# Optimization experiments

Hardware: AMD Instinct MI355X
Metric: run time of the kernel (lower is better)

The kernel has to match this reference:

```python
import jax, jax.numpy as jnp
from jax import lax
import numpy as np

B, DM, NL, NC = 4, 256, 4, 1000
DI, NS, DTR, K = 512, 16, 32, 4  # d_inner, d_state, dt_rank, d_conv
EPS = 1e-5


def _bn(x, g, b):
    # eval-mode BatchNorm2d with running stats (mean=0, var=1)
    return x * (g / jnp.sqrt(1.0 + EPS))[None, :, None, None] + b[None, :, None, None]


def _conv2d(x, w, b, stride, pad):
    y = lax.conv_general_dilated(x, w, (stride, stride), pad,
                                 dimension_numbers=('NCHW', 'OIHW', 'NCHW'))
    return y + b[None, :, None, None]


def _ln(x, g, b):
    m = x.mean(-1, keepdims=True)
    v = ((x - m) ** 2).mean(-1, keepdims=True)
    return (x - m) / jnp.sqrt(v + EPS) * g + b


def _selective_scan(u, delta, A, Bm, Cm, D):
    # u, delta: [b,d,l]; A: [d,n]; Bm, Cm: [b,n,l]; D: [d]
    dA = jnp.exp(jnp.einsum('bdl,dn->lbdn', delta, A))        # [l,b,d,n]
    dBu = jnp.einsum('bdl,bnl,bdl->lbdn', delta, Bm, u)       # [l,b,d,n]
    h0 = jnp.zeros(dA.shape[1:], u.dtype)

    def step(h, inp):
        a, bu = inp
        h = a * h + bu
        return h, h

    _, hs = lax.scan(step, h0, (dA, dBu))                     # [l,b,d,n]
    y = jnp.einsum('lbdn,bnl->bdl', hs, Cm)
    return y + u * D[None, :, None]


def _mamba_block(x, ipw, ipb, cw, cb, xpw, dpw, dpb, alog, dssm, opw, opb):
    # x: [b,l,d_model]
    xr = x @ ipw.T + ipb                                      # [b,l,2*DI]
    xi, res = jnp.split(xr, 2, axis=-1)
    xc = jnp.swapaxes(xi, 1, 2)                               # [b,DI,l]
    # depthwise conv1d, kernel 4, torch padding='same' -> pad (1,2)
    xc = lax.conv_general_dilated(xc, cw, (1,), [(1, 2)],
                                  dimension_numbers=('NCW', 'OIW', 'NCW'),
                                  feature_group_count=DI) + cb[None, :, None]
    xl = jnp.swapaxes(xc, 1, 2)                               # [b,l,DI]
    xdbl = xl @ xpw.T                                         # [b,l,DTR+2*NS]
    d_dt, Bs, Cs = jnp.split(xdbl, [DTR, DTR + NS], axis=-1)
    delta = jax.nn.softplus(d_dt @ dpw.T + dpb)               # [b,l,DI]
    A = -jnp.exp(alog)                                        # [DI,NS]
    y = _selective_scan(jnp.swapaxes(xl, 1, 2), jnp.swapaxes(delta, 1, 2), A,
                        jnp.swapaxes(Bs, 1, 2), jnp.swapaxes(Cs, 1, 2), dssm)
    y = jnp.swapaxes(y, 1, 2)                                 # [b,l,DI]
    y = y * jax.nn.silu(res)
    return y @ opw.T + opb


def setup_inputs() -> dict:
    key = jax.random.key(0)
    ks = iter(jax.random.split(key, 32))

    def rn(shape, scale=0.02):
        return jax.random.normal(next(ks), shape, jnp.float32) * scale

    inp = {
        'x': jax.random.normal(next(ks), (B, 3, 64, 64), jnp.float32),
        # conv stem
        'c1w': rn((DM // 2, 3, 3, 3)), 'c1b': jnp.zeros((DM // 2,)),
        'g1': jnp.ones((DM // 2,)), 'b1': jnp.zeros((DM // 2,)),
        'c2w': rn((DM, DM // 2, 3, 3)), 'c2b': jnp.zeros((DM,)),
        'g2': jnp.ones((DM,)), 'b2': jnp.zeros((DM,)),
        'pw': rn((DM, DM, 2, 2)), 'pb': jnp.zeros((DM,)),
        'g3': jnp.ones((DM,)), 'b3': jnp.zeros((DM,)),
        # stacked mamba block params [NL, ...]
        'ipw': rn((NL, 2 * DI, DM)), 'ipb': jnp.zeros((NL, 2 * DI)),
        'cw': rn((NL, DI, 1, K), 0.1), 'cb': jnp.zeros((NL, DI)),
        'xpw': rn((NL, DTR + 2 * NS, DI)),
        'dpw': rn((NL, DI, DTR)), 'dpb': rn((NL, DI), 0.1),
        'alog': jnp.broadcast_to(jnp.log(jnp.arange(1, NS + 1, dtype=jnp.float32)), (NL, DI, NS)),
        'dssm': jnp.ones((NL, DI)),
        'opw': rn((NL, DM, DI)), 'opb': jnp.zeros((NL, DM)),
        'lnw': jnp.ones((NL, DM)), 'lnb': jnp.zeros((NL, DM)),
        # head
        'nw': jnp.ones((DM,)), 'nb': jnp.zeros((DM,)),
        'fcw': rn((NC, DM)), 'fcb': jnp.zeros((NC,)),
    }
    return inp


def reference(x, c1w, c1b, g1, b1, c2w, c2b, g2, b2, pw, pb, g3, b3,
              ipw, ipb, cw, cb, xpw, dpw, dpb, alog, dssm, opw, opb,
              lnw, lnb, nw, nb, fcw, fcb):
    h = _conv2d(x, c1w, c1b, 1, [(1, 1), (1, 1)])
    h = jax.nn.gelu(_bn(h, g1, b1), approximate=False)
    h = _conv2d(h, c2w, c2b, 1, [(1, 1), (1, 1)])
    h = jax.nn.gelu(_bn(h, g2, b2), approximate=False)
    h = _conv2d(h, pw, pb, 2, [(0, 0), (0, 0)])
    h = jax.nn.gelu(_bn(h, g3, b3), approximate=False)
    b, c, H, W = h.shape
    s = h.reshape(b, c, H * W).transpose(0, 2, 1)             # [b, L, d_model]
    for i in range(NL):
        y = _mamba_block(s, ipw[i], ipb[i], cw[i], cb[i], xpw[i], dpw[i],
                         dpb[i], alog[i], dssm[i], opw[i], opb[i])
        s = _ln(y, lnw[i], lnb[i]) + s
    s = s.mean(axis=1)
    s = _ln(s, nw, nb)
    logits = s @ fcw.T + fcb
    return logits, jax.nn.softmax(logits, axis=-1)
```

## Files before the change

kernel.cpp:

```cpp
#include <hip/hip_runtime.h>
#include <math.h>


#define BN_RSQ 0.99999500003749969f

typedef unsigned int uint;
typedef unsigned short ushort;
typedef __bf16 bf16x8 __attribute__((ext_vector_type(8)));
typedef float floatx4 __attribute__((ext_vector_type(4)));

__device__ __forceinline__ float gelu_f(float v) {
    return 0.5f * v * (1.0f + erff(v * 0.70710678118654752f));
}
__device__ __forceinline__ float softplus_f(float v) {
    return (v > 20.f) ? v : log1pf(expf(v));
}
__device__ __forceinline__ ushort f2bf(float f) {
    uint x = __float_as_uint(f);
    x += 0x7fffu + ((x >> 16) & 1u);
    return (ushort)(x >> 16);
}
__device__ __forceinline__ float bf2f(ushort u) {
    return __uint_as_float((uint)u << 16);
}

__global__ void wprep(const float* __restrict__ ipw, const float* __restrict__ opw,
                      const float* __restrict__ c2w, const float* __restrict__ pw,
                      const float* __restrict__ xpw,
                      ushort* __restrict__ ipwb, ushort* __restrict__ opwb,
                      ushort* __restrict__ w2b, ushort* __restrict__ pwTb,
                      ushort* __restrict__ xpwb)
{
    int idx = blockIdx.x * 256 + threadIdx.x;
    if (idx < 1048576) {
        ipwb[idx] = f2bf(ipw[idx]);
    } else if (idx < 1572864) {
        int i = idx - 1048576;
        opwb[i] = f2bf(opw[i]);
    } else if (idx < 1867776) {
        int i = idx - 1572864;
        int oc = i / 1152, k = i % 1152;
        int s = k >> 7, ic = k & 127;
        w2b[i] = f2bf(c2w[(size_t)(oc * 128 + ic) * 9 + s]);
    } else if (idx < 2129920) {
        int i = idx - 1867776;
        int oc = i >> 10, k = i & 1023;
        int s = k >> 8, ic = k & 255;
        int ky = s >> 1, kx = s & 1;
        pwTb[i] = f2bf(pw[((size_t)(oc * 256 + ic) * 2 + ky) * 2 + kx]);
    } else if (idx < 2260992) {
        int i = idx - 2129920;
        xpwb[i] = f2bf(xpw[i]);
    }
}

__global__ __launch_bounds__(256) void conv1_nhwc(
    const float* __restrict__ x, const float* __restrict__ w,
    const float* __restrict__ cb, const float* __restrict__ g,
    const float* __restrict__ bb, ushort* __restrict__ out)
{
    __shared__ float tin[3][3][64];
    __shared__ float ws[3456];
    int t = threadIdx.x;
    int b = blockIdx.x >> 6, y = blockIdx.x & 63;
    for (int i = t; i < 3456; i += 256) ws[i] = w[i];
    for (int i = t; i < 576; i += 256) {
        int ic = i / 192, r = (i >> 6) % 3, xx = i & 63;
        int gy = y + r - 1;
        tin[ic][r][xx] = ((unsigned)gy < 64u) ? x[((b * 3 + ic) * 64 + gy) * 64 + xx] : 0.f;
    }
    __syncthreads();
    int tx = t & 15, ty = t >> 4;
    int oc0 = tx * 8, px0 = ty * 4;
    float acc[4][8];
    #pragma unroll
    for (int p = 0; p < 4; ++p)
        #pragma unroll
        for (int o = 0; o < 8; ++o) acc[p][o] = 0.f;
    for (int ic = 0; ic < 3; ++ic)
        #pragma unroll
        for (int ky = 0; ky < 3; ++ky)
            #pragma unroll
            for (int kx = 0; kx < 3; ++kx) {
                float av[4];
                #pragma unroll
                for (int p = 0; p < 4; ++p) {
                    int xx = px0 + p + kx - 1;
                    av[p] = ((unsigned)xx < 64u) ? tin[ic][ky][xx] : 0.f;
                }
                #pragma unroll
                for (int o = 0; o < 8; ++o) {
                    float wv = ws[(oc0 + o) * 27 + ic * 9 + ky * 3 + kx];
                    #pragma unroll
                    for (int p = 0; p < 4; ++p) acc[p][o] = fmaf(av[p], wv, acc[p][o]);
                }
            }
    #pragma unroll
    for (int p = 0; p < 4; ++p) {
        uint pk[4];
        #pragma unroll
        for (int o2 = 0; o2 < 4; ++o2) {
            int oc = oc0 + o2 * 2;
            float v0 = gelu_f((acc[p][o2 * 2] + cb[oc]) * (g[oc] * BN_RSQ) + bb[oc]);
            float v1 = gelu_f((acc[p][o2 * 2 + 1] + cb[oc + 1]) * (g[oc + 1] * BN_RSQ) + bb[oc + 1]);
            pk[o2] = (uint)f2bf(v0) | ((uint)f2bf(v1) << 16);
        }
        uint4 vv = make_uint4(pk[0], pk[1], pk[2], pk[3]);
        *(uint4*)(out + ((size_t)((b * 64 + y) * 64 + px0 + p)) * 128 + oc0) = vv;
    }
}

template<int BM, int BN, int EPI>
__global__ __launch_bounds__(256, 2) void mfma_gemm_bt(
    const ushort* __restrict__ A, int lda,
    const ushort* __restrict__ W, int ldw,
    const float* __restrict__ bias,
    const float* __restrict__ bnG, const float* __restrict__ bnB,
    float* __restrict__ Cf, ushort* __restrict__ Cb, ushort* __restrict__ Cb2,
    int ldc, int K)
{
    constexpr int PAD = 40;
    constexpr int AP = BM / 64;
    constexpr int BP = BN / 64;
    constexpr int FM = BM / 32;
    constexpr int FN = BN / 32;
    __shared__ __align__(16) ushort As[BM * PAD];
    __shared__ __align__(16) ushort Bs[BN * PAD];
    int t = threadIdx.x;
    int m0 = blockIdx.x * BM, n0 = blockIdx.y * BN;
    int lane = t & 63, wid = t >> 6;
    int wm = (wid & 1) * (BM / 2), wn = (wid >> 1) * (BN / 2);
    int fr = lane & 15, fk = (lane >> 4) * 8;
    int r0 = t >> 2, c0 = (t & 3) * 8;
    floatx4 acc[FM][FN];
    #pragma unroll
    for (int i = 0; i < FM; ++i)
        #pragma unroll
        for (int j = 0; j < FN; ++j) acc[i][j] = {0.f, 0.f, 0.f, 0.f};
    uint4 ra[AP], rb[BP];
    #pragma unroll
    for (int p = 0; p < AP; ++p)
        ra[p] = *(const uint4*)(A + (size_t)(m0 + r0 + p * 64) * lda + c0);
    #pragma unroll
    for (int p = 0; p < BP; ++p)
        rb[p] = *(const uint4*)(W + (size_t)(n0 + r0 + p * 64) * ldw + c0);
    for (int k0 = 0; k0 < K; k0 += 32) {
        __syncthreads();
        #pragma unroll
        for (int p = 0; p < AP; ++p) *(uint4*)&As[(r0 + p * 64) * PAD + c0] = ra[p];
        #pragma unroll
        for (int p = 0; p < BP; ++p) *(uint4*)&Bs[(r0 + p * 64) * PAD + c0] = rb[p];
        __syncthreads();
        if (k0 + 32 < K) {
            #pragma unroll
            for (int p = 0; p < AP; ++p)
                ra[p] = *(const uint4*)(A + (size_t)(m0 + r0 + p * 64) * lda + k0 + 32 + c0);
            #pragma unroll
            for (int p = 0; p < BP; ++p)
                rb[p] = *(const uint4*)(W + (size_t)(n0 + r0 + p * 64) * ldw + k0 + 32 + c0);
        }
        bf16x8 af[FM], bw[FN];
        #pragma unroll
        for (int i = 0; i < FM; ++i)
            af[i] = *(const bf16x8*)&As[(wm + i * 16 + fr) * PAD + fk];
        #pragma unroll
        for (int j = 0; j < FN; ++j)
            bw[j] = *(const bf16x8*)&Bs[(wn + j * 16 + fr) * PAD + fk];
        #pragma unroll
        for (int i = 0; i < FM; ++i)
            #pragma unroll
            for (int j = 0; j < FN; ++j)
                acc[i][j] = __builtin_amdgcn_mfma_f32_16x16x32_bf16(af[i], bw[j], acc[i][j], 0, 0, 0);
    }
    int rbase = (lane >> 4) * 4, cc = lane & 15;
    #pragma unroll
    for (int j = 0; j < FN; ++j) {
        int n = n0 + wn + j * 16 + cc;
        float bv = bias ? bias[n] : 0.f;
        float scl = 0.f, shf = 0.f;
        if (EPI == 2) { scl = bnG[n] * BN_RSQ; shf = bnB[n]; }
        #pragma unroll
        for (int i = 0; i < FM; ++i) {
            #pragma unroll
            for (int r = 0; r < 4; ++r) {
                int m = m0 + wm + i * 16 + rbase + r;
                float v = acc[i][j][r] + bv;
                if (EPI == 2) v = gelu_f(v * scl + shf);
                if (EPI == 0) {
                    Cf[(size_t)m * ldc + n] = v;
                } else if (EPI == 2) {
                    Cf[(size_t)m * ldc + n] = v;
                    Cb[(size_t)m * ldc + n] = f2bf(v);
                } else {
                    if (n < 512) Cb[(size_t)m * 512 + n] = f2bf(v);
                    else Cb2[(size_t)m * 512 + (n - 512)] = f2bf(v / (1.f + __expf(-v)));
                }
            }
        }
    }
}

#define C2_LOAD(step)                                                            \
    {                                                                            \
        int s_ = (step) >> 1, ich_ = ((step) & 1) * 64;                          \
        int ky_ = s_ / 3, kx_ = s_ % 3;                                          \
        int sy_ = y0 + (ra_row >> 6) + ky_ - 1;                                  \
        int sx_ = (ra_row & 63) + kx_ - 1;                                       \
        bool v_ = ((unsigned)sy_ < 64u) && ((unsigned)sx_ < 64u);                \
        const ushort* ap_ = hb + ((size_t)(sy_ * 64 + sx_)) * 128 + ich_ + ra_c; \
        uint4 zz_ = make_uint4(0u, 0u, 0u, 0u);                                  \
        ra0 = v_ ? *(const uint4*)(ap_ + 0)  : zz_;                              \
        ra1 = v_ ? *(const uint4*)(ap_ + 8)  : zz_;                              \
        ra2 = v_ ? *(const uint4*)(ap_ + 16) : zz_;                              \
        ra3 = v_ ? *(const uint4*)(ap_ + 24) : zz_;                              \
        const ushort* wp_ = w2b + (size_t)(n0 + rb_row) * 1152 + s_ * 128 + ich_ + rb_c; \
        rb0 = *(const uint4*)(wp_ + 0);                                          \
        rb1 = *(const uint4*)(wp_ + 8);                                          \
    }

__global__ __launch_bounds__(256, 2) void conv2_mfma(
    const ushort* __restrict__ h1b, const ushort* __restrict__ w2b,
    const float* __restrict__ cb, const float* __restrict__ g,
    const float* __restrict__ bb, ushort* __restrict__ h2b)
{
    constexpr int PAD = 72;
    __shared__ __align__(16) ushort As[128 * PAD];
    __shared__ __align__(16) ushort Bs[64 * PAD];
    int t = threadIdx.x;
    int m0 = blockIdx.x * 128, n0 = blockIdx.y * 64;
    int b = m0 >> 12;
    int y0 = (m0 & 4095) >> 6;
    int lane = t & 63, wid = t >> 6;
    int wm = (wid & 1) * 64, wn = (wid >> 1) * 32;
    int fr = lane & 15, fk = (lane >> 4) * 8;
    int ra_row = t >> 1, ra_c = (t & 1) * 32;
    int rb_row = t >> 2, rb_c = (t & 3) * 16;
    floatx4 acc[4][2];
    #pragma unroll
    for (int i = 0; i < 4; ++i)
        #pragma unroll
        for (int j = 0; j < 2; ++j) acc[i][j] = {0.f, 0.f, 0.f, 0.f};
    const ushort* hb = h1b + (size_t)b * 4096 * 128;

    uint4 ra0, ra1, ra2, ra3, rb0, rb1;
    C2_LOAD(0);
    for (int step = 0; step < 18; ++step) {
        __syncthreads();
        *(uint4*)&As[ra_row * PAD + ra_c + 0]  = ra0;
        *(uint4*)&As[ra_row * PAD + ra_c + 8]  = ra1;
        *(uint4*)&As[ra_row * PAD + ra_c + 16] = ra2;
        *(uint4*)&As[ra_row * PAD + ra_c + 24] = ra3;
        *(uint4*)&Bs[rb_row * PAD + rb_c + 0]  = rb0;
        *(uint4*)&Bs[rb_row * PAD + rb_c + 8]  = rb1;
        __syncthreads();
        if (step + 1 < 18) C2_LOAD(step + 1);
        #pragma unroll
        for (int ks = 0; ks < 64; ks += 32) {
            bf16x8 af[4], bw[2];
            #pragma unroll
            for (int i = 0; i < 4; ++i)
                af[i] = *(const bf16x8*)&As[(wm + i * 16 + fr) * PAD + ks + fk];
            #pragma unroll
            for (int j = 0; j < 2; ++j)
                bw[j] = *(const bf16x8*)&Bs[(wn + j * 16 + fr) * PAD + ks + fk];
            #pragma unroll
            for (int i = 0; i < 4; ++i)
                #pragma unroll
                for (int j = 0; j < 2; ++j)
                    acc[i][j] = __builtin_amdgcn_mfma_f32_16x16x32_bf16(af[i], bw[j], acc[i][j], 0, 0, 0);
        }
    }
    int rbase = (lane >> 4) * 4, cc = lane & 15;
    #pragma unroll
    for (int j = 0; j < 2; ++j) {
        int n = n0 + wn + j * 16 + cc;
        float scl = g[n] * BN_RSQ, shf = bb[n], bv2 = cb[n];
        #pragma unroll
        for (int i = 0; i < 4; ++i) {
            #pragma unroll
            for (int r = 0; r < 4; ++r) {
                int m = m0 + wm + i * 16 + rbase + r;
                float v = gelu_f((acc[i][j][r] + bv2) * scl + shf);
                h2b[(size_t)m * 256 + n] = f2bf(v);
            }
        }
    }
}

__global__ void im2col_bf16(const ushort* __restrict__ h2b, ushort* __restrict__ Apb)
{
    int idx = blockIdx.x * 256 + threadIdx.x;
    int k8 = idx & 127;
    int m = idx >> 7;
    int b = m >> 10, oy = (m >> 5) & 31, ox = m & 31;
    int s = k8 >> 5, ic8 = k8 & 31;
    int ky = s >> 1, kx = s & 1;
    uint4 v = *(const uint4*)(h2b + ((size_t)(b * 4096 + (2 * oy + ky) * 64 + 2 * ox + kx)) * 256 + ic8 * 8);
    *(uint4*)(Apb + (size_t)m * 1024 + k8 * 8) = v;
}

template<int BM, int BN, int BK, int TM, int TN>
__global__ __launch_bounds__(256) void gemm_kernel(
    const float* __restrict__ A, int lda,
    const float* __restrict__ W, int ldw,
    const float* __restrict__ bias,
    float* __restrict__ C, int ldc,
    int M, int N, int K, int act)
{
    static_assert(BM * BK / 4 == 256 && BN * BK / 4 == 256, "staging shape");
    __shared__ float As[BK][BM + 4];
    __shared__ float Bs[BK][BN + 4];
    int t = threadIdx.x;
    int m0 = blockIdx.x * BM, n0 = blockIdx.y * BN;
    float acc[TM][TN];
    #pragma unroll
    for (int i = 0; i < TM; i++)
        #pragma unroll
        for (int j = 0; j < TN; j++) acc[i][j] = 0.f;
    const int LPR = BK / 4;
    int lr = t / LPR, lc4 = (t % LPR) * 4;
    int ty = t >> 4, tx = t & 15;
    int ma = m0 + lr, nb = n0 + lr;
    float4 va = make_float4(0.f, 0.f, 0.f, 0.f);
    float4 vb = make_float4(0.f, 0.f, 0.f, 0.f);
    if (ma < M) va = *(const float4*)(A + (size_t)ma * lda + lc4);
    if (nb < N) vb = *(const float4*)(W + (size_t)nb * ldw + lc4);
    for (int k0 = 0; k0 < K; k0 += BK) {
        __syncthreads();
        As[lc4 + 0][lr] = va.x; As[lc4 + 1][lr] = va.y;
        As[lc4 + 2][lr] = va.z; As[lc4 + 3][lr] = va.w;
        Bs[lc4 + 0][lr] = vb.x; Bs[lc4 + 1][lr] = vb.y;
        Bs[lc4 + 2][lr] = vb.z; Bs[lc4 + 3][lr] = vb.w;
        __syncthreads();
        if (k0 + BK < K) {
            if (ma < M) va = *(const float4*)(A + (size_t)ma * lda + k0 + BK + lc4);
            if (nb < N) vb = *(const float4*)(W + (size_t)nb * ldw + k0 + BK + lc4);
        }
        #pragma unroll
        for (int kk = 0; kk < BK; ++kk) {
            float a[TM], bfr[TN];
            #pragma unroll
            for (int i = 0; i < TM; i += 4)
                *(float4*)&a[i] = *(const float4*)&As[kk][ty * TM + i];
            #pragma unroll
            for (int j = 0; j < TN; j += 4)
                *(float4*)&bfr[j] = *(const float4*)&Bs[kk][tx * TN + j];
            #pragma unroll
            for (int i = 0; i < TM; i++)
                #pragma unroll
                for (int j = 0; j < TN; j++) acc[i][j] = fmaf(a[i], bfr[j], acc[i][j]);
        }
    }
    #pragma unroll
    for (int i = 0; i < TM; i++) {
        int m = m0 + ty * TM + i;
        if (m >= M) continue;
        #pragma unroll
        for (int j = 0; j < TN; j++) {
            int n = n0 + tx * TN + j;
            if (n >= N) continue;
            float v = acc[i][j];
            if (bias) v += bias[n];
            if (act == 2) v = softplus_f(v);
            C[(size_t)m * ldc + n] = v;
        }
    }
}

__global__ __launch_bounds__(256) void dwconv(
    const ushort* __restrict__ xib, const float* __restrict__ cw,
    const float* __restrict__ cb, float* __restrict__ xl, ushort* __restrict__ xlb)
{
    int idx = blockIdx.x * 256 + threadIdx.x;
    int d4 = (idx & 127) * 4;
    int bl = idx >> 7;
    int b = bl >> 10, l = bl & 1023;
    float4 w0 = *(const float4*)(cw + d4 * 4);
    float4 w1 = *(const float4*)(cw + d4 * 4 + 4);
    float4 w2 = *(const float4*)(cw + d4 * 4 + 8);
    float4 w3 = *(const float4*)(cw + d4 * 4 + 12);
    float4 acc = *(const float4*)(cb + d4);
    const ushort* rowb = xib + ((size_t)b << 19) + d4;
    #pragma unroll
    for (int k = 0; k < 4; ++k) {
        int ll = l + k - 1;
        if ((unsigned)ll < 1024u) {
            uint2 p = *(const uint2*)(rowb + (size_t)ll * 512);
            acc.x = fmaf(bf2f((ushort)(p.x & 0xffffu)), ((const float*)&w0)[k], acc.x);
            acc.y = fmaf(bf2f((ushort)(p.x >> 16)),     ((const float*)&w1)[k], acc.y);
            acc.z = fmaf(bf2f((ushort)(p.y & 0xffffu)), ((const float*)&w2)[k], acc.z);
            acc.w = fmaf(bf2f((ushort)(p.y >> 16)),     ((const float*)&w3)[k], acc.w);
        }
    }
    *(float4*)(xl + (size_t)bl * 512 + d4) = acc;
    uint2 pk;
    pk.x = (uint)f2bf(acc.x) | ((uint)f2bf(acc.y) << 16);
    pk.y = (uint)f2bf(acc.z) | ((uint)f2bf(acc.w) << 16);
    *(uint2*)(xlb + (size_t)bl * 512 + d4) = pk;
}

__global__ __launch_bounds__(512) void scan_part1(
    const float* __restrict__ delta, const float* __restrict__ u,
    const float* __restrict__ xdbl, const float* __restrict__ alog,
    float* __restrict__ Psum, float* __restrict__ hFsum)
{
    __shared__ float Td[32][132];
    __shared__ float Tu[32][132];
    __shared__ float TB[16][132];
    int t = threadIdx.x;
    int bid = blockIdx.x;
    int ch = bid & 7, dgG = (bid >> 3) & 15, b = bid >> 7;
    int d0 = dgG * 32;
    int bl0 = b * 1024 + ch * 128;
    #pragma unroll
    for (int r = 0; r < 2; ++r) {
        int idx = r * 512 + t;
        int l = idx >> 3, d4 = (idx & 7) * 4;
        float4 dv = *(const float4*)(delta + (size_t)(bl0 + l) * 512 + d0 + d4);
        float4 uv = *(const float4*)(u + (size_t)(bl0 + l) * 512 + d0 + d4);
        Td[d4 + 0][l] = dv.x; Td[d4 + 1][l] = dv.y; Td[d4 + 2][l] = dv.z; Td[d4 + 3][l] = dv.w;
        Tu[d4 + 0][l] = uv.x; Tu[d4 + 1][l] = uv.y; Tu[d4 + 2][l] = uv.z; Tu[d4 + 3][l] = uv.w;
    }
    {
        int l = t >> 2, n4 = (t & 3) * 4;
        float4 bv = *(const float4*)(xdbl + (size_t)(bl0 + l) * 64 + 32 + n4);
        TB[n4 + 0][l] = bv.x; TB[n4 + 1][l] = bv.y; TB[n4 + 2][l] = bv.z; TB[n4 + 3][l] = bv.w;
    }
    __syncthreads();
    int w = t >> 6, lane = t & 63;
    int dl = lane >> 4, n = lane & 15;
    int col = w * 4 + dl;
    int d = d0 + col;
    float Ac = -__expf(alog[d * 16 + n]);
    float h = 0.f, P = 1.f;
    for (int l4 = 0; l4 < 32; ++l4) {
        float4 de = *(const float4*)&Td[col][l4 * 4];
        float4 uu = *(const float4*)&Tu[col][l4 * 4];
        float4 Bv = *(const float4*)&TB[n][l4 * 4];
        float a;
        a = __expf(de.x * Ac); h = a * h + de.x * Bv.x * uu.x; P *= a;
        a = __expf(de.y * Ac); h = a * h + de.y * Bv.y * uu.y; P *= a;
        a = __expf(de.z * Ac); h = a * h + de.z * Bv.z * uu.z; P *= a;
        a = __expf(de.w * Ac); h = a * h + de.w * Bv.w * uu.w; P *= a;
    }
    size_t si = ((size_t)(b * 128 + dgG * 8 + w) * 8 + ch) * 64 + lane;
    Psum[si] = P;
    hFsum[si] = h;
}

__global__ __launch_bounds__(512) void scan_part2(
    const float* __restrict__ delta, const float* __restrict__ u,
    const float* __restrict__ xdbl,
    const float* __restrict__ alog, const float* __restrict__ dssm,
    const ushort* __restrict__ resb, ushort* __restrict__ ybb,
    const float* __restrict__ Psum, const float* __restrict__ hFsum)
{
    __shared__ float Td[32][132];
    __shared__ float Tu[32][132];
    __shared__ float TB[16][132];
    __shared__ float TC[16][132];
    __shared__ float yb[128][33];
    int t = threadIdx.x;
    int bid = blockIdx.x;
    int ch = bid & 7, dgG = (bid >> 3) & 15, b = bid >> 7;
    int d0 = dgG * 32;
    int bl0 = b * 1024 + ch * 128;
    #pragma unroll
    for (int r = 0; r < 2; ++r) {
        int idx = r * 512 + t;
        int l = idx >> 3, d4 = (idx & 7) * 4;
        float4 dv = *(const float4*)(delta + (size_t)(bl0 + l) * 512 + d0 + d4);
        float4 uv = *(const float4*)(u + (size_t)(bl0 + l) * 512 + d0 + d4);
        Td[d4 + 0][l] = dv.x; Td[d4 + 1][l] = dv.y; Td[d4 + 2][l] = dv.z; Td[d4 + 3][l] = dv.w;
        Tu[d4 + 0][l] = uv.x; Tu[d4 + 1][l] = uv.y; Tu[d4 + 2][l] = uv.z; Tu[d4 + 3][l] = uv.w;
    }
    {
        int l = t >> 2, n4 = (t & 3) * 4;
        float4 bv = *(const float4*)(xdbl + (size_t)(bl0 + l) * 64 + 32 + n4);
        float4 cv = *(const float4*)(xdbl + (size_t)(bl0 + l) * 64 + 48 + n4);
        TB[n4 + 0][l] = bv.x; TB[n4 + 1][l] = bv.y; TB[n4 + 2][l] = bv.z; TB[n4 + 3][l] = bv.w;
        TC[n4 + 0][l] = cv.x; TC[n4 + 1][l] = cv.y; TC[n4 + 2][l] = cv.z; TC[n4 + 3][l] = cv.w;
    }
    __syncthreads();
    int w = t >> 6, lane = t & 63;
    int dl = lane >> 4, n = lane & 15;
    int col = w * 4 + dl;
    int d = d0 + col;
    float Ac = -__expf(alog[d * 16 + n]);
    float Dd = dssm[d];
    float h = 0.f;
    {
        size_t sbase = (size_t)(b * 128 + dgG * 8 + w) * 512 + lane;
        for (int cc = 0; cc < ch; ++cc) {
            float Pv = Psum[sbase + (size_t)cc * 64];
            float hv = hFsum[sbase + (size_t)cc * 64];
            h = Pv * h + hv;
        }
    }
    for (int l4 = 0; l4 < 32; ++l4) {
        float4 de = *(const float4*)&Td[col][l4 * 4];
        float4 uu = *(const float4*)&Tu[col][l4 * 4];
        float4 Bv = *(const float4*)&TB[n][l4 * 4];
        float4 Cv = *(const float4*)&TC[n][l4 * 4];
        float p0, p1, p2, p3;
        h = __expf(de.x * Ac) * h + de.x * Bv.x * uu.x; p0 = h * Cv.x;
        h = __expf(de.y * Ac) * h + de.y * Bv.y * uu.y; p1 = h * Cv.y;
        h = __expf(de.z * Ac) * h + de.z * Bv.z * uu.z; p2 = h * Cv.z;
        h = __expf(de.w * Ac) * h + de.w * Bv.w * uu.w; p3 = h * Cv.w;
        #pragma unroll
        for (int off = 1; off < 16; off <<= 1) {
            p0 += __shfl_xor(p0, off);
            p1 += __shfl_xor(p1, off);
            p2 += __shfl_xor(p2, off);
            p3 += __shfl_xor(p3, off);
        }
        if (n == 0) {
            int l = l4 * 4;
            yb[l + 0][col] = fmaf(uu.x, Dd, p0);
            yb[l + 1][col] = fmaf(uu.y, Dd, p1);
            yb[l + 2][col] = fmaf(uu.z, Dd, p2);
            yb[l + 3][col] = fmaf(uu.w, Dd, p3);
        }
    }
    __syncthreads();
    size_t base = ((size_t)(b * 1024 + ch * 128)) * 512 + d0;
    const uint* rp32 = (const uint*)(resb + base);
    uint* yp32 = (uint*)(ybb + base);
    #pragma unroll
    for (int j = 0; j < 4; ++j) {
        int idx = j * 512 + t;
        int l = idx >> 4, du = idx & 15;
        float v0 = yb[l][du * 2 + 0];
        float v1 = yb[l][du * 2 + 1];
        uint rr = rp32[(size_t)l * 256 + du];
        float y0 = v0 * bf2f((ushort)(rr & 0xffffu));
        float y1 = v1 * bf2f((ushort)(rr >> 16));
        yp32[(size_t)l * 256 + du] = (uint)f2bf(y0) | ((uint)f2bf(y1) << 16);
    }
}

__global__ __launch_bounds__(256) void ln_res_kernel(
    const float* __restrict__ o, const float* __restrict__ g,
    const float* __restrict__ bb, float* __restrict__ s, ushort* __restrict__ sb)
{
    int row = blockIdx.x * 4 + (threadIdx.x >> 6);
    int lane = threadIdx.x & 63;
    const float4* orow = (const float4*)(o + (size_t)row * 256);
    float4 v = orow[lane];
    float sum = v.x + v.y + v.z + v.w;
    float sq = v.x * v.x + v.y * v.y + v.z * v.z + v.w * v.w;
    #pragma unroll
    for (int off = 1; off < 64; off <<= 1) {
        sum += __shfl_xor(sum, off);
        sq += __shfl_xor(sq, off);
    }
    float m = sum * (1.f / 256.f);
    float var = sq * (1.f / 256.f) - m * m;
    float rstd = rsqrtf(var + 1e-5f);
    float4 gg = ((const float4*)g)[lane];
    float4 bv = ((const float4*)bb)[lane];
    float4* srow = (float4*)(s + (size_t)row * 256);
    float4 sv = srow[lane];
    sv.x += (v.x - m) * rstd * gg.x + bv.x;
    sv.y += (v.y - m) * rstd * gg.y + bv.y;
    sv.z += (v.z - m) * rstd * gg.z + bv.z;
    sv.w += (v.w - m) * rstd * gg.w + bv.w;
    srow[lane] = sv;
    uint2 pk;
    pk.x = (uint)f2bf(sv.x) | ((uint)f2bf(sv.y) << 16);
    pk.y = (uint)f2bf(sv.z) | ((uint)f2bf(sv.w) << 16);
    *(uint2*)(sb + (size_t)row * 256 + lane * 4) = pk;
}

__global__ __launch_bounds__(256) void pool_ln_kernel(
    const float* __restrict__ s, const float* __restrict__ nw,
    const float* __restrict__ nb, float* __restrict__ sln)
{
    int b = blockIdx.x, c = threadIdx.x;
    const float* p = s + (size_t)b * 262144 + c;
    float acc = 0.f;
    for (int l = 0; l < 1024; ++l) acc += p[(size_t)l * 256];
    float pooled = acc * (1.f / 1024.f);
    __shared__ float rs[4], rq[4];
    float sum = pooled, sq = pooled * pooled;
    #pragma unroll
    for (int off = 1; off < 64; off <<= 1) {
        sum += __shfl_xor(sum, off);
        sq += __shfl_xor(sq, off);
    }
    int w = threadIdx.x >> 6;
    if ((threadIdx.x & 63) == 0) { rs[w] = sum; rq[w] = sq; }
    __syncthreads();
    sum = rs[0] + rs[1] + rs[2] + rs[3];
    sq = rq[0] + rq[1] + rq[2] + rq[3];
    float m = sum * (1.f / 256.f);
    float var = sq * (1.f / 256.f) - m * m;
    float rstd = rsqrtf(var + 1e-5f);
    sln[b * 256 + c] = (pooled - m) * rstd * nw[c] + nb[c];
}

__global__ __launch_bounds__(256) void softmax_kernel(float* __restrict__ out)
{
    int b = threadIdx.x >> 6, lane = threadIdx.x & 63;
    const float* lg = out + b * 1000;
    float v[16];
    float mx = -1e30f;
    #pragma unroll
    for (int j = 0; j < 16; ++j) {
        int i = lane + j * 64;
        v[j] = (i < 1000) ? lg[i] : -1e30f;
        mx = fmaxf(mx, v[j]);
    }
    #pragma unroll
    for (int off = 1; off < 64; off <<= 1) mx = fmaxf(mx, __shfl_xor(mx, off));
    float sum = 0.f;
    #pragma unroll
    for (int j = 0; j < 16; ++j) {
        int i = lane + j * 64;
        if (i < 1000) { v[j] = __expf(v[j] - mx); sum += v[j]; }
    }
    #pragma unroll
    for (int off = 1; off < 64; off <<= 1) sum += __shfl_xor(sum, off);
    float inv = 1.f / sum;
    float* so = out + 4000 + b * 1000;
    #pragma unroll
    for (int j = 0; j < 16; ++j) {
        int i = lane + j * 64;
        if (i < 1000) so[i] = v[j] * inv;
    }
}

extern "C" void kernel_launch(void* const* d_in, const int* in_sizes, int n_in,
                              void* d_out, int out_size, void* d_ws, size_t ws_size,
                              hipStream_t stream)
{
    const float* x    = (const float*)d_in[0];
    const float* c1w  = (const float*)d_in[1];
    const float* c1b  = (const float*)d_in[2];
    const float* g1   = (const float*)d_in[3];
    const float* b1   = (const float*)d_in[4];
    const float* c2w  = (const float*)d_in[5];
    const float* c2b  = (const float*)d_in[6];
    const float* g2   = (const float*)d_in[7];
    const float* b2   = (const float*)d_in[8];
    const float* pw   = (const float*)d_in[9];
    const float* pb   = (const float*)d_in[10];
    const float* g3   = (const float*)d_in[11];
    const float* b3   = (const float*)d_in[12];
    const float* ipw  = (const float*)d_in[13];
    const float* ipb  = (const float*)d_in[14];
    const float* cw   = (const float*)d_in[15];
    const float* cb   = (const float*)d_in[16];
    const float* xpw  = (const float*)d_in[17];
    const float* dpw  = (const float*)d_in[18];
    const float* dpb  = (const float*)d_in[19];
    const float* alog = (const float*)d_in[20];
    const float* dssm = (const float*)d_in[21];
    const float* opw  = (const float*)d_in[22];
    const float* opb  = (const float*)d_in[23];
    const float* lnw  = (const float*)d_in[24];
    const float* lnb  = (const float*)d_in[25];
    const float* nw   = (const float*)d_in[26];
    const float* nb   = (const float*)d_in[27];
    const float* fcw  = (const float*)d_in[28];
    const float* fcb  = (const float*)d_in[29];
    float* out = (float*)d_out;
    float* wsf = (float*)d_ws;

    float*  s_   = wsf;
    ushort* sb   = (ushort*)(wsf + 1048576);
    ushort* xib  = (ushort*)(wsf + 1572864);
    ushort* h2b  = (ushort*)(wsf + 1572864);
    float*  delta= wsf + 1572864;
    float*  obuf = wsf + 1572864;
    ushort* resb = (ushort*)(wsf + 3670016);
    ushort* xlb  = (ushort*)(wsf + 4718592);
    ushort* ybb  = (ushort*)(wsf + 4718592);
    ushort* h1b  = (ushort*)(wsf + 4718592);
    float*  xl   = wsf + 6815744;
    ushort* Apb  = (ushort*)(wsf + 6815744);
    float*  xdbl = wsf + 8912896;
    ushort* ipwb = (ushort*)(wsf + 9175040);
    ushort* opwb = (ushort*)(wsf + 9699328);
    ushort* w2b  = (ushort*)(wsf + 9961472);
    ushort* pwTb = (ushort*)(wsf + 10108928);
    float*  sln  = wsf + 10240000;
    float*  Psum = wsf + 10241024;
    float*  hFsum= wsf + 10503168;
    ushort* xpwb = (ushort*)(wsf + 10765312);

    hipLaunchKernelGGL(wprep, dim3(8832), dim3(256), 0, stream,
                       ipw, opw, c2w, pw, xpw, ipwb, opwb, w2b, pwTb, xpwb);

    hipLaunchKernelGGL(conv1_nhwc, dim3(256), dim3(256), 0, stream, x, c1w, c1b, g1, b1, h1b);
    hipLaunchKernelGGL(conv2_mfma, dim3(128, 4), dim3(256), 0, stream, h1b, w2b, c2b, g2, b2, h2b);
    hipLaunchKernelGGL(im2col_bf16, dim3(2048), dim3(256), 0, stream, h2b, Apb);
    hipLaunchKernelGGL((mfma_gemm_bt<64, 64, 2>), dim3(64, 4), dim3(256), 0, stream,
                       Apb, 1024, pwTb, 1024, pb, g3, b3, s_, sb, nullptr, 256, 1024);

    for (int i = 0; i < 4; ++i) {
        const ushort* ipwb_i = ipwb + (size_t)i * 1024 * 256;
        const float*  ipb_i  = ipb + i * 1024;
        const float*  cw_i   = cw + i * 512 * 4;
        const float*  cb_i   = cb + i * 512;
        const ushort* xpwb_i = xpwb + (size_t)i * 64 * 512;
        const float*  dpw_i  = dpw + (size_t)i * 512 * 32;
        const float*  dpb_i  = dpb + i * 512;
        const float*  alog_i = alog + (size_t)i * 512 * 16;
        const float*  dssm_i = dssm + i * 512;
        const ushort* opwb_i = opwb + (size_t)i * 256 * 512;
        const float*  opb_i  = opb + i * 256;
        const float*  lnw_i  = lnw + i * 256;
        const float*  lnb_i  = lnb + i * 256;

        hipLaunchKernelGGL((mfma_gemm_bt<64, 128, 3>), dim3(64, 8), dim3(256), 0, stream,
                           sb, 256, ipwb_i, 256, ipb_i, nullptr, nullptr,
                           nullptr, xib, resb, 0, 256);
        hipLaunchKernelGGL(dwconv, dim3(2048), dim3(256), 0, stream, xib, cw_i, cb_i, xl, xlb);
        hipLaunchKernelGGL((mfma_gemm_bt<64, 64, 0>), dim3(64, 1), dim3(256), 0, stream,
                           xlb, 512, xpwb_i, 512, nullptr, nullptr, nullptr,
                           xdbl, nullptr, nullptr, 64, 512);
        hipLaunchKernelGGL((gemm_kernel<64, 64, 16, 4, 4>), dim3(64, 8), dim3(256), 0, stream,
                           xdbl, 64, dpw_i, 32, dpb_i, delta, 512, 4096, 512, 32, 2);
        hipLaunchKernelGGL(scan_part1, dim3(512), dim3(512), 0, stream,
                           delta, xl, xdbl, alog_i, Psum, hFsum);
        hipLaunchKernelGGL(scan_part2, dim3(512), dim3(512), 0, stream,
                           delta, xl, xdbl, alog_i, dssm_i, resb, ybb, Psum, hFsum);
        hipLaunchKernelGGL((mfma_gemm_bt<64, 64, 0>), dim3(64, 4), dim3(256), 0, stream,
                           ybb, 512, opwb_i, 512, opb_i, nullptr, nullptr,
                           obuf, nullptr, nullptr, 256, 512);
        hipLaunchKernelGGL(ln_res_kernel, dim3(1024), dim3(256), 0, stream,
                           obuf, lnw_i, lnb_i, s_, sb);
    }

    hipLaunchKernelGGL(pool_ln_kernel, dim3(4), dim3(256), 0, stream, s_, nw, nb, sln);
    hipLaunchKernelGGL((gemm_kernel<64, 64, 16, 4, 4>), dim3(1, 16), dim3(256), 0, stream,
                       sln, 256, fcw, 256, fcb, out, 1000, 4, 1000, 256, 0);
    hipLaunchKernelGGL(softmax_kernel, dim3(1), dim3(256), 0, stream, out);
}
```

Before: 670.1 us.

## Fuse dt_proj GEMM and softplus into scan kernels and read u as bf16

Drops the separate dt_proj GEMM that wrote a float delta tensor. Both scan kernels now recompute delta per tile from xdbl and dpw held in shared memory, then apply softplus. The scan input u is read from the bf16 conv output instead of a float copy, so dwconv no longer writes the float xl buffer. This removes one launch per layer and a lot of global traffic, but the delta projection is computed twice (once per scan pass) and u loses precision to bf16.

```diff
diff --git a/kernel.cpp b/kernel.cpp
--- a/kernel.cpp
+++ b/kernel.cpp
@@ -369,7 +369,7 @@
 
 __global__ __launch_bounds__(256) void dwconv(
     const ushort* __restrict__ xib, const float* __restrict__ cw,
-    const float* __restrict__ cb, float* __restrict__ xl, ushort* __restrict__ xlb)
+    const float* __restrict__ cb, ushort* __restrict__ xlb)
 {
     int idx = blockIdx.x * 256 + threadIdx.x;
     int d4 = (idx & 127) * 4;
@@ -392,7 +392,6 @@
             acc.w = fmaf(bf2f((ushort)(p.y >> 16)),     ((const float*)&w3)[k], acc.w);
         }
     }
-    *(float4*)(xl + (size_t)bl * 512 + d4) = acc;
     uint2 pk;
     pk.x = (uint)f2bf(acc.x) | ((uint)f2bf(acc.y) << 16);
     pk.y = (uint)f2bf(acc.z) | ((uint)f2bf(acc.w) << 16);
@@ -400,13 +399,17 @@
 }
 
 __global__ __launch_bounds__(512) void scan_part1(
-    const float* __restrict__ delta, const float* __restrict__ u,
-    const float* __restrict__ xdbl, const float* __restrict__ alog,
+    const float* __restrict__ xdbl, const ushort* __restrict__ xlb,
+    const float* __restrict__ dpw, const float* __restrict__ dpb,
+    const float* __restrict__ alog,
     float* __restrict__ Psum, float* __restrict__ hFsum)
 {
     __shared__ float Td[32][132];
     __shared__ float Tu[32][132];
     __shared__ float TB[16][132];
+    __shared__ float xd[128][32];
+    __shared__ float dpw_s[32][33];
+    __shared__ float dpb_s[32];
     int t = threadIdx.x;
     int bid = blockIdx.x;
     int ch = bid & 7, dgG = (bid >> 3) & 15, b = bid >> 7;
@@ -415,16 +418,45 @@
     #pragma unroll
     for (int r = 0; r < 2; ++r) {
         int idx = r * 512 + t;
-        int l = idx >> 3, d4 = (idx & 7) * 4;
-        float4 dv = *(const float4*)(delta + (size_t)(bl0 + l) * 512 + d0 + d4);
-        float4 uv = *(const float4*)(u + (size_t)(bl0 + l) * 512 + d0 + d4);
-        Td[d4 + 0][l] = dv.x; Td[d4 + 1][l] = dv.y; Td[d4 + 2][l] = dv.z; Td[d4 + 3][l] = dv.w;
-        Tu[d4 + 0][l] = uv.x; Tu[d4 + 1][l] = uv.y; Tu[d4 + 2][l] = uv.z; Tu[d4 + 3][l] = uv.w;
+        int l = idx >> 3, k4 = (idx & 7) * 4;
+        float4 v = *(const float4*)(xdbl + (size_t)(bl0 + l) * 64 + k4);
+        *(float4*)&xd[l][k4] = v;
+    }
+    {
+        int l = t >> 2, d8 = (t & 3) * 8;
+        uint4 p = *(const uint4*)(xlb + (size_t)(bl0 + l) * 512 + d0 + d8);
+        Tu[d8 + 0][l] = bf2f((ushort)(p.x & 0xffffu));
+        Tu[d8 + 1][l] = bf2f((ushort)(p.x >> 16));
+        Tu[d8 + 2][l] = bf2f((ushort)(p.y & 0xffffu));
+        Tu[d8 + 3][l] = bf2f((ushort)(p.y >> 16));
+        Tu[d8 + 4][l] = bf2f((ushort)(p.z & 0xffffu));
+        Tu[d8 + 5][l] = bf2f((ushort)(p.z >> 16));
+        Tu[d8 + 6][l] = bf2f((ushort)(p.w & 0xffffu));
+        Tu[d8 + 7][l] = bf2f((ushort)(p.w >> 16));
     }
     {
         int l = t >> 2, n4 = (t & 3) * 4;
         float4 bv = *(const float4*)(xdbl + (size_t)(bl0 + l) * 64 + 32 + n4);
         TB[n4 + 0][l] = bv.x; TB[n4 + 1][l] = bv.y; TB[n4 + 2][l] = bv.z; TB[n4 + 3][l] = bv.w;
+    }
+    #pragma unroll
+    for (int r = 0; r < 2; ++r) {
+        int idx = r * 512 + t;
+        int dd = idx >> 5, kk = idx & 31;
+        dpw_s[dd][kk] = dpw[(size_t)(d0 + dd) * 32 + kk];
+    }
+    if (t < 32) dpb_s[t] = dpb[d0 + t];
+    __syncthreads();
+    {
+        int dd = t & 31, lb = (t >> 5) * 8;
+        #pragma unroll
+        for (int j = 0; j < 8; ++j) {
+            int l = lb + j;
+            float s = dpb_s[dd];
+            #pragma unroll
+            for (int k = 0; k < 32; ++k) s = fmaf(xd[l][k], dpw_s[dd][k], s);
+            Td[dd][l] = softplus_f(s);
+        }
     }
     __syncthreads();
     int w = t >> 6, lane = t & 63;
@@ -449,8 +481,8 @@
 }
 
 __global__ __launch_bounds__(512) void scan_part2(
-    const float* __restrict__ delta, const float* __restrict__ u,
-    const float* __restrict__ xdbl,
+    const float* __restrict__ xdbl, const ushort* __restrict__ xlb,
+    const float* __restrict__ dpw, const float* __restrict__ dpb,
     const float* __restrict__ alog, const float* __restrict__ dssm,
     const ushort* __restrict__ resb, ushort* __restrict__ ybb,
     const float* __restrict__ Psum, const float* __restrict__ hFsum)
@@ -460,6 +492,8 @@
     __shared__ float TB[16][132];
     __shared__ float TC[16][132];
     __shared__ float yb[128][33];
+    __shared__ float dpw_s[32][33];
+    __shared__ float dpb_s[32];
     int t = threadIdx.x;
     int bid = blockIdx.x;
     int ch = bid & 7, dgG = (bid >> 3) & 15, b = bid >> 7;
@@ -468,11 +502,21 @@
     #pragma unroll
     for (int r = 0; r < 2; ++r) {
         int idx = r * 512 + t;
-        int l = idx >> 3, d4 = (idx & 7) * 4;
-        float4 dv = *(const float4*)(delta + (size_t)(bl0 + l) * 512 + d0 + d4);
-        float4 uv = *(const float4*)(u + (size_t)(bl0 + l) * 512 + d0 + d4);
-        Td[d4 + 0][l] = dv.x; Td[d4 + 1][l] = dv.y; Td[d4 + 2][l] = dv.z; Td[d4 + 3][l] = dv.w;
-        Tu[d4 + 0][l] = uv.x; Tu[d4 + 1][l] = uv.y; Tu[d4 + 2][l] = uv.z; Tu[d4 + 3][l] = uv.w;
+        int l = idx >> 3, k4 = (idx & 7) * 4;
+        float4 v = *(const float4*)(xdbl + (size_t)(bl0 + l) * 64 + k4);
+        *(float4*)&yb[l][k4] = v;
+    }
+    {
+        int l = t >> 2, d8 = (t & 3) * 8;
+        uint4 p = *(const uint4*)(xlb + (size_t)(bl0 + l) * 512 + d0 + d8);
+        Tu[d8 + 0][l] = bf2f((ushort)(p.x & 0xffffu));
+        Tu[d8 + 1][l] = bf2f((ushort)(p.x >> 16));
+        Tu[d8 + 2][l] = bf2f((ushort)(p.y & 0xffffu));
+        Tu[d8 + 3][l] = bf2f((ushort)(p.y >> 16));
+        Tu[d8 + 4][l] = bf2f((ushort)(p.z & 0xffffu));
+        Tu[d8 + 5][l] = bf2f((ushort)(p.z >> 16));
+        Tu[d8 + 6][l] = bf2f((ushort)(p.w & 0xffffu));
+        Tu[d8 + 7][l] = bf2f((ushort)(p.w >> 16));
     }
     {
         int l = t >> 2, n4 = (t & 3) * 4;
@@ -481,7 +525,25 @@
         TB[n4 + 0][l] = bv.x; TB[n4 + 1][l] = bv.y; TB[n4 + 2][l] = bv.z; TB[n4 + 3][l] = bv.w;
         TC[n4 + 0][l] = cv.x; TC[n4 + 1][l] = cv.y; TC[n4 + 2][l] = cv.z; TC[n4 + 3][l] = cv.w;
     }
+    #pragma unroll
+    for (int r = 0; r < 2; ++r) {
+        int idx = r * 512 + t;
+        int dd = idx >> 5, kk = idx & 31;
+        dpw_s[dd][kk] = dpw[(size_t)(d0 + dd) * 32 + kk];
+    }
+    if (t < 32) dpb_s[t] = dpb[d0 + t];
     __syncthreads();
+    {
+        int dd = t & 31, lb = (t >> 5) * 8;
+        #pragma unroll
+        for (int j = 0; j < 8; ++j) {
+            int l = lb + j;
+            float s = dpb_s[dd];
+            #pragma unroll
+            for (int k = 0; k < 32; ++k) s = fmaf(yb[l][k], dpw_s[dd][k], s);
+            Td[dd][l] = softplus_f(s);
+        }
+    }
     int w = t >> 6, lane = t & 63;
     int dl = lane >> 4, n = lane & 15;
     int col = w * 4 + dl;
@@ -497,6 +559,7 @@
             h = Pv * h + hv;
         }
     }
+    __syncthreads();
     for (int l4 = 0; l4 < 32; ++l4) {
         float4 de = *(const float4*)&Td[col][l4 * 4];
         float4 uu = *(const float4*)&Tu[col][l4 * 4];
@@ -671,13 +734,11 @@
     ushort* sb   = (ushort*)(wsf + 1048576);
     ushort* xib  = (ushort*)(wsf + 1572864);
     ushort* h2b  = (ushort*)(wsf + 1572864);
-    float*  delta= wsf + 1572864;
     float*  obuf = wsf + 1572864;
     ushort* resb = (ushort*)(wsf + 3670016);
     ushort* xlb  = (ushort*)(wsf + 4718592);
     ushort* ybb  = (ushort*)(wsf + 4718592);
     ushort* h1b  = (ushort*)(wsf + 4718592);
-    float*  xl   = wsf + 6815744;
     ushort* Apb  = (ushort*)(wsf + 6815744);
     float*  xdbl = wsf + 8912896;
     ushort* ipwb = (ushort*)(wsf + 9175040);
@@ -716,16 +777,14 @@
         hipLaunchKernelGGL((mfma_gemm_bt<64, 128, 3>), dim3(64, 8), dim3(256), 0, stream,
                            sb, 256, ipwb_i, 256, ipb_i, nullptr, nullptr,
                            nullptr, xib, resb, 0, 256);
-        hipLaunchKernelGGL(dwconv, dim3(2048), dim3(256), 0, stream, xib, cw_i, cb_i, xl, xlb);
+        hipLaunchKernelGGL(dwconv, dim3(2048), dim3(256), 0, stream, xib, cw_i, cb_i, xlb);
         hipLaunchKernelGGL((mfma_gemm_bt<64, 64, 0>), dim3(64, 1), dim3(256), 0, stream,
                            xlb, 512, xpwb_i, 512, nullptr, nullptr, nullptr,
                            xdbl, nullptr, nullptr, 64, 512);
-        hipLaunchKernelGGL((gemm_kernel<64, 64, 16, 4, 4>), dim3(64, 8), dim3(256), 0, stream,
-                           xdbl, 64, dpw_i, 32, dpb_i, delta, 512, 4096, 512, 32, 2);
         hipLaunchKernelGGL(scan_part1, dim3(512), dim3(512), 0, stream,
-                           delta, xl, xdbl, alog_i, Psum, hFsum);
+                           xdbl, xlb, dpw_i, dpb_i, alog_i, Psum, hFsum);
         hipLaunchKernelGGL(scan_part2, dim3(512), dim3(512), 0, stream,
-                           delta, xl, xdbl, alog_i, dssm_i, resb, ybb, Psum, hFsum);
+                           xdbl, xlb, dpw_i, dpb_i, alog_i, dssm_i, resb, ybb, Psum, hFsum);
         hipLaunchKernelGGL((mfma_gemm_bt<64, 64, 0>), dim3(64, 4), dim3(256), 0, stream,
                            ybb, 512, opwb_i, 512, opb_i, nullptr, nullptr,
                            obuf, nullptr, nullptr, 256, 512);
```

Result: faster. 655.8 us (-2.1%).
